# Performance work log

Hardware: AMD Instinct MI355X
Metric: run time of the kernel (lower is better)

Reference implementation:

```python
import jax, jax.numpy as jnp
import numpy as np
from jax import lax

B, C_IN, C_OUT, KS, K, FD, L = 32, 128, 256, 9, 8, 64, 4096
PAD = KS // 2


def setup_inputs() -> dict:
    key = jax.random.key(0)
    ks = jax.random.split(key, 8)
    X = jax.random.normal(ks[0], (B, C_IN, L), dtype=jnp.float32)
    Z = jax.random.normal(ks[1], (B, FD), dtype=jnp.float32)
    # z_to_in: Linear(fluct_dim, in_planes), xavier-ish init, zero bias
    z_in_w = jax.random.normal(ks[2], (C_IN, FD), dtype=jnp.float32) * (1.0 / np.sqrt(FD))
    z_in_b = jnp.zeros((C_IN,), dtype=jnp.float32)
    # z_to_w MLP: in_planes -> in_planes//2 -> K
    w1 = jax.random.normal(ks[3], (C_IN // 2, C_IN), dtype=jnp.float32) * (1.0 / np.sqrt(C_IN))
    b1 = jax.random.normal(ks[4], (C_IN // 2,), dtype=jnp.float32) * 0.01
    w2 = jax.random.normal(ks[5], (K, C_IN // 2), dtype=jnp.float32) * (1.0 / np.sqrt(C_IN // 2))
    b2 = jax.random.normal(ks[6], (K,), dtype=jnp.float32) * 0.01
    weight_bank = jax.random.normal(ks[7], (K, C_OUT, C_IN, KS), dtype=jnp.float32) * (1.0 / np.sqrt(C_IN * KS))
    bias_bank = jnp.zeros((K, C_OUT), dtype=jnp.float32)
    return {"X": X, "Z": Z, "z_in_w": z_in_w, "z_in_b": z_in_b,
            "w1": w1, "b1": b1, "w2": w2, "b2": b2,
            "weight_bank": weight_bank, "bias_bank": bias_bank}


def _conv_one(x, w):
    # x: (C_in, L); w: (C_out, C_in, KS) -> (C_out, L)
    y = lax.conv_general_dilated(x[None], w, window_strides=(1,),
                                 padding=[(PAD, PAD)],
                                 dimension_numbers=("NCH", "OIH", "NCH"))
    return y[0]


def reference(X, Z, z_in_w, z_in_b, w1, b1, w2, b2, weight_bank, bias_bank):
    # routing: Z -> in_planes -> MLP -> softmax over K (dropout is inference no-op)
    proj = Z @ z_in_w.T + z_in_b                       # (B, C_in)
    h = jax.nn.relu(proj @ w1.T + b1)                  # (B, C_in//2)
    logits = h @ w2.T + b2                             # (B, K)
    omega = jax.nn.softmax(logits, axis=1)             # (B, K)
    # per-sample mixed kernels and biases
    W_tilde = jnp.einsum("bk,koci->boci", omega, weight_bank)  # (B, C_out, C_in, KS)
    b_tilde = omega @ bias_bank                         # (B, C_out)
    # batched per-sample conv (equiv. of the groups=B conv1d trick)
    Y = jax.vmap(_conv_one)(X, W_tilde)                 # (B, C_out, L)
    return Y + b_tilde[:, :, None]
```

## Files before the change

kernel.cpp:

```cpp
#include <hip/hip_runtime.h>
#include <math.h>

#define B_     32
#define C_INP  128
#define C_OUTP 256
#define KS_    9
#define KK_    8
#define FD_    64
#define LL_    4096
#define PAD_   4

#define LPAD   (LL_ + 2 * PAD_)

typedef unsigned short ushort_t;
typedef short bf16x8 __attribute__((ext_vector_type(8)));
typedef float f32x4 __attribute__((ext_vector_type(4)));

__device__ __forceinline__ ushort_t f2bf(float f) {
    unsigned u = __float_as_uint(f);
    unsigned r = (u + 0x7FFFu + ((u >> 16) & 1u)) >> 16;
    return (ushort_t)r;
}

__device__ __forceinline__ void gload16(const void* g, void* l) {
    __builtin_amdgcn_global_load_lds(
        (const __attribute__((address_space(1))) unsigned int*)g,
        (__attribute__((address_space(3))) unsigned int*)l, 16, 0, 0);
}

__global__ __launch_bounds__(256) void routing_kernel(
    const float* __restrict__ Z, const float* __restrict__ z_in_w,
    const float* __restrict__ z_in_b, const float* __restrict__ w1,
    const float* __restrict__ b1, const float* __restrict__ w2,
    const float* __restrict__ b2, const float* __restrict__ bias_bank,
    float* __restrict__ omega_out, float* __restrict__ btilde_out)
{
    const int b = blockIdx.x;
    const int tid = threadIdx.x;
    __shared__ float s_z[FD_];
    __shared__ float s_proj[C_INP];
    __shared__ float s_h[FD_];
    __shared__ float s_logits[KK_];
    __shared__ float s_omega[KK_];

    if (tid < FD_) s_z[tid] = Z[b * FD_ + tid];
    __syncthreads();

    if (tid < C_INP) {
        float acc = z_in_b[tid];
        const float* w = z_in_w + tid * FD_;
        #pragma unroll 8
        for (int f = 0; f < FD_; ++f) acc = fmaf(w[f], s_z[f], acc);
        s_proj[tid] = acc;
    }
    __syncthreads();

    if (tid < FD_) {
        float acc = b1[tid];
        const float* w = w1 + tid * C_INP;
        #pragma unroll 8
        for (int c = 0; c < C_INP; ++c) acc = fmaf(w[c], s_proj[c], acc);
        s_h[tid] = fmaxf(acc, 0.0f);
    }
    __syncthreads();

    if (tid < KK_) {
        float acc = b2[tid];
        const float* w = w2 + tid * FD_;
        #pragma unroll 8
        for (int j = 0; j < FD_; ++j) acc = fmaf(w[j], s_h[j], acc);
        s_logits[tid] = acc;
    }
    __syncthreads();

    if (tid == 0) {
        float m = s_logits[0];
        #pragma unroll
        for (int k = 1; k < KK_; ++k) m = fmaxf(m, s_logits[k]);
        float e[KK_];
        float s = 0.0f;
        #pragma unroll
        for (int k = 0; k < KK_; ++k) { e[k] = expf(s_logits[k] - m); s += e[k]; }
        const float inv = 1.0f / s;
        #pragma unroll
        for (int k = 0; k < KK_; ++k) s_omega[k] = e[k] * inv;
    }
    __syncthreads();

    if (tid < KK_) omega_out[b * KK_ + tid] = s_omega[tid];

    {
        float acc = 0.0f;
        #pragma unroll
        for (int k = 0; k < KK_; ++k) acc = fmaf(s_omega[k], bias_bank[k * C_OUTP + tid], acc);
        btilde_out[b * C_OUTP + tid] = acc;
    }
}

__global__ __launch_bounds__(256) void mix_kernel(
    const float* __restrict__ bank, const float* __restrict__ omega,
    ushort_t* __restrict__ wt)
{
    __shared__ float s_bank[KK_ * C_INP * KS_];
    __shared__ float s_om[B_ * KK_];

    const int o = blockIdx.x;
    const int tid = threadIdx.x;

    s_om[tid] = omega[tid];
    #pragma unroll
    for (int k = 0; k < KK_; ++k) {
        const float* src = bank + ((size_t)(k * C_OUTP + o)) * (C_INP * KS_);
        for (int i = tid; i < C_INP * KS_; i += 256)
            s_bank[k * (C_INP * KS_) + i] = src[i];
    }
    __syncthreads();

    for (int j = tid; j < KS_ * (C_INP / 2); j += 256) {
        const int t = j >> 6;
        const int c = (j & 63) * 2;
        float v0[KK_], v1[KK_];
        #pragma unroll
        for (int k = 0; k < KK_; ++k) {
            v0[k] = s_bank[k * (C_INP * KS_) + c * KS_ + t];
            v1[k] = s_bank[k * (C_INP * KS_) + (c + 1) * KS_ + t];
        }
        #pragma unroll
        for (int b = 0; b < B_; ++b) {
            float a0 = 0.0f, a1 = 0.0f;
            #pragma unroll
            for (int k = 0; k < KK_; ++k) {
                const float om = s_om[b * KK_ + k];
                a0 = fmaf(om, v0[k], a0);
                a1 = fmaf(om, v1[k], a1);
            }
            const unsigned packed = (unsigned)f2bf(a0) | ((unsigned)f2bf(a1) << 16);
            *(unsigned*)&wt[(((size_t)b * KS_ + t) * C_OUTP + o) * C_INP + c] = packed;
        }
    }
}

__global__ __launch_bounds__(256) void transpose_kernel(
    const float* __restrict__ X, ushort_t* __restrict__ XT)
{
    __shared__ ushort_t s_t[64 * 130];

    const int tid = threadIdx.x;
    const int l0 = blockIdx.x * 64;
    const int b = blockIdx.y;

    const int ll = tid & 63;
    const int cq = tid >> 6;
    const float* xb = X + ((size_t)b * C_INP) * LL_;

    #pragma unroll 4
    for (int r = 0; r < 32; ++r) {
        const int c = r * 4 + cq;
        s_t[ll * 130 + c] = f2bf(xb[(size_t)c * LL_ + l0 + ll]);
    }
    __syncthreads();

    ushort_t* xtb = XT + (size_t)b * LPAD * C_INP;
    for (int it = tid; it < 64 * 64; it += 256) {
        const int row = it >> 6;
        const int p = it & 63;
        const unsigned lo = s_t[row * 130 + p * 2];
        const unsigned hi = s_t[row * 130 + p * 2 + 1];
        *(unsigned*)(xtb + ((size_t)(4 + l0 + row)) * C_INP + p * 2) = lo | (hi << 16);
    }
    if (l0 == 0) {
        const int row = tid >> 6, p = tid & 63;
        *(unsigned*)(xtb + (size_t)row * C_INP + p * 2) = 0u;
    }
    if (l0 == LL_ - 64) {
        const int row = tid >> 6, p = tid & 63;
        *(unsigned*)(xtb + ((size_t)(LL_ + PAD_ + row)) * C_INP + p * 2) = 0u;
    }
}

__global__ __launch_bounds__(256) void gemm_kernel(
    const ushort_t* __restrict__ XT, const ushort_t* __restrict__ WT,
    const float* __restrict__ btilde, float* __restrict__ Y)
{
    __shared__ __align__(16) ushort_t sX[136 * 128];
    __shared__ __align__(16) ushort_t sW[128 * 128];

    const int tid = threadIdx.x;
    const int wid = tid >> 6;
    const int lane = tid & 63;

    const int wg = blockIdx.x;
    const int logical = (wg & 7) * 256 + (wg >> 3);
    const int b  = logical >> 6;
    const int rem = logical & 63;
    const int o0 = (rem >> 5) << 7;
    const int l0 = (rem & 31) << 7;

    const int prow = lane >> 4;
    const int pcol = lane & 15;

    const ushort_t* xsrc = XT + ((size_t)b * LPAD + l0) * C_INP;
    for (int ci = wid; ci < 34; ci += 4) {
        const int row = ci * 4 + prow;
        const int scol = pcol ^ (row & 7);
        gload16(xsrc + row * C_INP + scol * 8, sX + ci * 512 + lane * 8);
    }

    {
        const ushort_t* wsrc = WT + (((size_t)b * KS_ + 0) * C_OUTP + o0) * C_INP;
        for (int ci = wid; ci < 32; ci += 4) {
            const int row = ci * 4 + prow;
            const int scol = pcol ^ (row & 7);
            gload16(wsrc + row * C_INP + scol * 8, sW + ci * 512 + lane * 8);
        }
    }
    __syncthreads();

    const int ln15 = lane & 15;
    const int lh = lane >> 4;
    const int wm0 = (wid >> 1) * 64;
    const int wn0 = (wid & 1) * 64;

    f32x4 acc[4][4];
    #pragma unroll
    for (int i = 0; i < 4; ++i)
        #pragma unroll
        for (int j = 0; j < 4; ++j) acc[i][j] = (f32x4){0.f, 0.f, 0.f, 0.f};

    for (int t = 0; t < KS_; ++t) {
        const int xrow0 = wn0 + t + ln15;
        #pragma unroll
        for (int kk = 0; kk < 4; ++kk) {
            const int col16 = kk * 4 + lh;
            bf16x8 a[4], bx[4];
            #pragma unroll
            for (int i = 0; i < 4; ++i) {
                const int arow = wm0 + i * 16 + ln15;
                a[i] = *(const bf16x8*)&sW[(arow << 7) + ((col16 ^ (arow & 7)) << 3)];
            }
            #pragma unroll
            for (int j = 0; j < 4; ++j) {
                const int brow = xrow0 + j * 16;
                bx[j] = *(const bf16x8*)&sX[(brow << 7) + ((col16 ^ (brow & 7)) << 3)];
            }
            #pragma unroll
            for (int i = 0; i < 4; ++i)
                #pragma unroll
                for (int j = 0; j < 4; ++j)
                    acc[i][j] = __builtin_amdgcn_mfma_f32_16x16x32_bf16(
                        a[i], bx[j], acc[i][j], 0, 0, 0);
        }
        __syncthreads();
        if (t < KS_ - 1) {
            const ushort_t* wsrc = WT + (((size_t)b * KS_ + (t + 1)) * C_OUTP + o0) * C_INP;
            for (int ci = wid; ci < 32; ci += 4) {
                const int row = ci * 4 + prow;
                const int scol = pcol ^ (row & 7);
                gload16(wsrc + row * C_INP + scol * 8, sW + ci * 512 + lane * 8);
            }
            __syncthreads();
        }
    }

    #pragma unroll
    for (int i = 0; i < 4; ++i) {
        const int obase = o0 + wm0 + i * 16 + lh * 4;
        const float4 bt = *(const float4*)&btilde[b * C_OUTP + obase];
        #pragma unroll
        for (int j = 0; j < 4; ++j) {
            const int lcol = l0 + wn0 + j * 16 + ln15;
            float* yp = Y + ((size_t)(b * C_OUTP + obase)) * LL_ + lcol;
            yp[0]           = acc[i][j][0] + bt.x;
            yp[LL_]         = acc[i][j][1] + bt.y;
            yp[2 * LL_]     = acc[i][j][2] + bt.z;
            yp[3 * LL_]     = acc[i][j][3] + bt.w;
        }
    }
}

#define O_TILE 8
#define T_PAD  12
__global__ __launch_bounds__(256) void conv_kernel(
    const float* __restrict__ X, const float* __restrict__ bank,
    const float* __restrict__ omega, const float* __restrict__ btilde,
    float* __restrict__ Y)
{
    __shared__ __align__(16) float s_w[C_INP * O_TILE * T_PAD];
    __shared__ float s_om[KK_];

    const int tid = threadIdx.x;
    const int o_base = blockIdx.x * O_TILE;
    const int b = blockIdx.y;

    if (tid < KK_) s_om[tid] = omega[b * KK_ + tid];
    __syncthreads();

    {
        const size_t kstride = (size_t)C_OUTP * C_INP * KS_;
        const float* bank_base = bank + (size_t)o_base * C_INP * KS_;
        for (int idx = tid; idx < O_TILE * C_INP * KS_; idx += 256) {
            const int o = idx / (C_INP * KS_);
            const int rem = idx - o * (C_INP * KS_);
            const int c = rem / KS_;
            const int t = rem - c * KS_;
            const float* p = bank_base + idx;
            float acc = 0.0f;
            #pragma unroll
            for (int k = 0; k < KK_; ++k) acc = fmaf(s_om[k], p[k * kstride], acc);
            s_w[(c * O_TILE + o) * T_PAD + t] = acc;
        }
    }
    __syncthreads();

    const int og = tid >> 7;
    const int lg = tid & 127;
    const float* xb = X + (size_t)b * C_INP * LL_;

    float bt[4];
    #pragma unroll
    for (int o = 0; o < 4; ++o) bt[o] = btilde[b * C_OUTP + o_base + og * 4 + o];

    for (int it = 0; it < 4; ++it) {
        const int l0 = it * 1024 + lg * 8;
        const int lx = l0 - PAD_;
        const bool fast = (lx >= 0) && (lx + 16 <= LL_);

        float acc[4][8];
        #pragma unroll
        for (int o = 0; o < 4; ++o)
            #pragma unroll
            for (int j = 0; j < 8; ++j) acc[o][j] = 0.0f;

        #pragma unroll 1
        for (int c = 0; c < C_INP; ++c) {
            const float* xrow = xb + (size_t)c * LL_;
            float x[16];
            if (fast) {
                const float4* p = reinterpret_cast<const float4*>(xrow + lx);
                const float4 a0 = p[0], a1 = p[1], a2 = p[2], a3 = p[3];
                x[0]=a0.x; x[1]=a0.y; x[2]=a0.z; x[3]=a0.w;
                x[4]=a1.x; x[5]=a1.y; x[6]=a1.z; x[7]=a1.w;
                x[8]=a2.x; x[9]=a2.y; x[10]=a2.z; x[11]=a2.w;
                x[12]=a3.x; x[13]=a3.y; x[14]=a3.z; x[15]=a3.w;
            } else {
                #pragma unroll
                for (int j = 0; j < 16; ++j) {
                    const int q = lx + j;
                    x[j] = (q >= 0 && q < LL_) ? xrow[q] : 0.0f;
                }
            }
            const float* wp = &s_w[(c * O_TILE + og * 4) * T_PAD];
            #pragma unroll
            for (int o = 0; o < 4; ++o) {
                #pragma unroll
                for (int t = 0; t < KS_; ++t) {
                    const float wv = wp[o * T_PAD + t];
                    #pragma unroll
                    for (int j = 0; j < 8; ++j)
                        acc[o][j] = fmaf(wv, x[j + t], acc[o][j]);
                }
            }
        }

        float* yb = Y + ((size_t)(b * C_OUTP + o_base + og * 4)) * LL_ + l0;
        #pragma unroll
        for (int o = 0; o < 4; ++o) {
            float4 r0, r1;
            r0.x = acc[o][0] + bt[o]; r0.y = acc[o][1] + bt[o];
            r0.z = acc[o][2] + bt[o]; r0.w = acc[o][3] + bt[o];
            r1.x = acc[o][4] + bt[o]; r1.y = acc[o][5] + bt[o];
            r1.z = acc[o][6] + bt[o]; r1.w = acc[o][7] + bt[o];
            float4* yp = reinterpret_cast<float4*>(yb + (size_t)o * LL_);
            yp[0] = r0; yp[1] = r1;
        }
    }
}

extern "C" void kernel_launch(void* const* d_in, const int* in_sizes, int n_in,
                              void* d_out, int out_size, void* d_ws, size_t ws_size,
                              hipStream_t stream)
{
    const float* X         = (const float*)d_in[0];
    const float* Z         = (const float*)d_in[1];
    const float* z_in_w    = (const float*)d_in[2];
    const float* z_in_b    = (const float*)d_in[3];
    const float* w1        = (const float*)d_in[4];
    const float* b1        = (const float*)d_in[5];
    const float* w2        = (const float*)d_in[6];
    const float* b2        = (const float*)d_in[7];
    const float* bank      = (const float*)d_in[8];
    const float* bias_bank = (const float*)d_in[9];
    float* out = (float*)d_out;

    char* ws = (char*)d_ws;
    float* omega  = (float*)ws;
    float* btilde = (float*)(ws + 1024);
    ushort_t* wt  = (ushort_t*)(ws + 1024 + 32768);
    ushort_t* XT  = (ushort_t*)(ws + 1024 + 32768 + (size_t)B_ * KS_ * C_OUTP * C_INP * 2);
    const size_t WS_NEEDED = 1024 + 32768
        + (size_t)B_ * KS_ * C_OUTP * C_INP * 2
        + (size_t)B_ * LPAD * C_INP * 2;

    routing_kernel<<<B_, 256, 0, stream>>>(Z, z_in_w, z_in_b, w1, b1, w2, b2,
                                           bias_bank, omega, btilde);

    if (ws_size >= WS_NEEDED) {
        mix_kernel<<<C_OUTP, 256, 0, stream>>>(bank, omega, wt);
        transpose_kernel<<<dim3(LL_ / 64, B_), 256, 0, stream>>>(X, XT);
        gemm_kernel<<<2048, 256, 0, stream>>>(XT, wt, btilde, out);
    } else {
        dim3 grid(C_OUTP / O_TILE, B_);
        conv_kernel<<<grid, 256, 0, stream>>>(X, bank, omega, btilde, out);
    }
}
```

Baseline: 136.4 us.

## Enlarge GEMM tile to 256x256 with double-buffered K-split weight loads

The implicit-GEMM conv kernel now uses 512-thread workgroups, each covering all 256 output channels by 256 positions, with a wave tile of 128x64. The reduction over input channels is split into two 64-wide halves, and the weight slice for the next step is prefetched into a second LDS buffer while the current step runs its MFMAs, which removes one barrier per tap. It also raises wave priority around the MFMA blocks. The aim is better data reuse and hiding load latency, at the cost of more accumulator registers (128 floats per lane), more LDS and fewer workgroups (512).

```diff
diff --git a/kernel.cpp b/kernel.cpp
--- a/kernel.cpp
+++ b/kernel.cpp
@@ -178,93 +178,112 @@
     }
 }
 
-__global__ __launch_bounds__(256) void gemm_kernel(
+__global__ __launch_bounds__(512, 2) void gemm_kernel(
     const ushort_t* __restrict__ XT, const ushort_t* __restrict__ WT,
     const float* __restrict__ btilde, float* __restrict__ Y)
 {
-    __shared__ __align__(16) ushort_t sX[136 * 128];
-    __shared__ __align__(16) ushort_t sW[128 * 128];
+    __shared__ __align__(16) ushort_t sW[2][256 * 64];
+    __shared__ __align__(16) ushort_t sX[2][264 * 64];
 
     const int tid = threadIdx.x;
     const int wid = tid >> 6;
     const int lane = tid & 63;
 
     const int wg = blockIdx.x;
-    const int logical = (wg & 7) * 256 + (wg >> 3);
-    const int b  = logical >> 6;
-    const int rem = logical & 63;
-    const int o0 = (rem >> 5) << 7;
-    const int l0 = (rem & 31) << 7;
-
-    const int prow = lane >> 4;
-    const int pcol = lane & 15;
-
-    const ushort_t* xsrc = XT + ((size_t)b * LPAD + l0) * C_INP;
-    for (int ci = wid; ci < 34; ci += 4) {
-        const int row = ci * 4 + prow;
-        const int scol = pcol ^ (row & 7);
-        gload16(xsrc + row * C_INP + scol * 8, sX + ci * 512 + lane * 8);
-    }
+    const int logical = (wg & 7) * 64 + (wg >> 3);
+    const int b  = logical >> 4;
+    const int l0 = (logical & 15) << 8;
 
     {
-        const ushort_t* wsrc = WT + (((size_t)b * KS_ + 0) * C_OUTP + o0) * C_INP;
-        for (int ci = wid; ci < 32; ci += 4) {
-            const int row = ci * 4 + prow;
-            const int scol = pcol ^ (row & 7);
-            gload16(wsrc + row * C_INP + scol * 8, sW + ci * 512 + lane * 8);
+        const ushort_t* xtb = XT + ((size_t)b * LPAD + l0) * C_INP;
+        #pragma unroll
+        for (int g0 = 0; g0 < 4224; g0 += 512) {
+            const int g = g0 + tid;
+            if (g < 4224) {
+                const int ch = g / 2112;
+                const int gg = g - ch * 2112;
+                const int row = gg >> 3;
+                const int pc = gg & 7;
+                const int scol = pc ^ (row & 7);
+                gload16(xtb + row * C_INP + ch * 64 + scol * 8,
+                        &sX[ch][0] + gg * 8);
+            }
+        }
+        const ushort_t* wbase = WT + (((size_t)b * KS_ + 0) * C_OUTP) * C_INP;
+        #pragma unroll
+        for (int it = 0; it < 4; ++it) {
+            const int g = it * 512 + tid;
+            const int row = g >> 3;
+            const int pc = g & 7;
+            const int scol = pc ^ (row & 7);
+            gload16(wbase + row * C_INP + scol * 8, &sW[0][0] + g * 8);
         }
     }
     __syncthreads();
 
     const int ln15 = lane & 15;
     const int lh = lane >> 4;
-    const int wm0 = (wid >> 1) * 64;
-    const int wn0 = (wid & 1) * 64;
-
-    f32x4 acc[4][4];
+    const int wm0 = (wid >> 2) * 128;
+    const int wn0 = (wid & 3) * 64;
+
+    f32x4 acc[8][4];
     #pragma unroll
-    for (int i = 0; i < 4; ++i)
+    for (int i = 0; i < 8; ++i)
         #pragma unroll
         for (int j = 0; j < 4; ++j) acc[i][j] = (f32x4){0.f, 0.f, 0.f, 0.f};
 
-    for (int t = 0; t < KS_; ++t) {
-        const int xrow0 = wn0 + t + ln15;
-        #pragma unroll
-        for (int kk = 0; kk < 4; ++kk) {
-            const int col16 = kk * 4 + lh;
-            bf16x8 a[4], bx[4];
-            #pragma unroll
-            for (int i = 0; i < 4; ++i) {
+    #pragma unroll 1
+    for (int s = 0; s < 2 * KS_; ++s) {
+        const int buf = s & 1;
+        const int t = s >> 1;
+        const int ch = s & 1;
+
+        if (s < 2 * KS_ - 1) {
+            const int s1 = s + 1;
+            const int t1 = s1 >> 1;
+            const int ch1 = s1 & 1;
+            const ushort_t* wbase =
+                WT + (((size_t)b * KS_ + t1) * C_OUTP) * C_INP + ch1 * 64;
+            #pragma unroll
+            for (int it = 0; it < 4; ++it) {
+                const int g = it * 512 + tid;
+                const int row = g >> 3;
+                const int pc = g & 7;
+                const int scol = pc ^ (row & 7);
+                gload16(wbase + row * C_INP + scol * 8, &sW[buf ^ 1][0] + g * 8);
+            }
+        }
+
+        const ushort_t* wh = &sW[buf][0];
+        const ushort_t* xh = &sX[ch][0];
+        #pragma unroll
+        for (int kk = 0; kk < 2; ++kk) {
+            bf16x8 a[8], bx[4];
+            #pragma unroll
+            for (int i = 0; i < 8; ++i) {
                 const int arow = wm0 + i * 16 + ln15;
-                a[i] = *(const bf16x8*)&sW[(arow << 7) + ((col16 ^ (arow & 7)) << 3)];
+                a[i] = *(const bf16x8*)&wh[arow * 64 + (((kk * 4 + lh) ^ (arow & 7)) << 3)];
             }
             #pragma unroll
             for (int j = 0; j < 4; ++j) {
-                const int brow = xrow0 + j * 16;
-                bx[j] = *(const bf16x8*)&sX[(brow << 7) + ((col16 ^ (brow & 7)) << 3)];
-            }
-            #pragma unroll
-            for (int i = 0; i < 4; ++i)
+                const int brow = wn0 + t + j * 16 + ln15;
+                bx[j] = *(const bf16x8*)&xh[brow * 64 + (((kk * 4 + lh) ^ (brow & 7)) << 3)];
+            }
+            __builtin_amdgcn_s_setprio(1);
+            #pragma unroll
+            for (int i = 0; i < 8; ++i)
                 #pragma unroll
                 for (int j = 0; j < 4; ++j)
                     acc[i][j] = __builtin_amdgcn_mfma_f32_16x16x32_bf16(
                         a[i], bx[j], acc[i][j], 0, 0, 0);
+            __builtin_amdgcn_s_setprio(0);
         }
         __syncthreads();
-        if (t < KS_ - 1) {
-            const ushort_t* wsrc = WT + (((size_t)b * KS_ + (t + 1)) * C_OUTP + o0) * C_INP;
-            for (int ci = wid; ci < 32; ci += 4) {
-                const int row = ci * 4 + prow;
-                const int scol = pcol ^ (row & 7);
-                gload16(wsrc + row * C_INP + scol * 8, sW + ci * 512 + lane * 8);
-            }
-            __syncthreads();
-        }
     }
 
     #pragma unroll
-    for (int i = 0; i < 4; ++i) {
-        const int obase = o0 + wm0 + i * 16 + lh * 4;
+    for (int i = 0; i < 8; ++i) {
+        const int obase = wm0 + i * 16 + lh * 4;
         const float4 bt = *(const float4*)&btilde[b * C_OUTP + obase];
         #pragma unroll
         for (int j = 0; j < 4; ++j) {
@@ -407,7 +426,7 @@
     if (ws_size >= WS_NEEDED) {
         mix_kernel<<<C_OUTP, 256, 0, stream>>>(bank, omega, wt);
         transpose_kernel<<<dim3(LL_ / 64, B_), 256, 0, stream>>>(X, XT);
-        gemm_kernel<<<2048, 256, 0, stream>>>(XT, wt, btilde, out);
+        gemm_kernel<<<512, 512, 0, stream>>>(XT, wt, btilde, out);
     } else {
         dim3 grid(C_OUTP / O_TILE, B_);
         conv_kernel<<<grid, 256, 0, stream>>>(X, bank, omega, btilde, out);
```

Result: no change. 137.1 us (+0.5%).

## Pipeline weight tiles through a four-slot LDS ring with prefetch depth three

Applied to the files above, without the earlier changes.

The weight tile is now split into 32-channel K-slices held in a four-slot shared-memory ring. Each loop step prefetches the slice three steps ahead with async global-to-LDS loads while MFMAs run on the current slice. This replaces the serial load/sync/compute per tap and its double barrier with one barrier plus a partial vmcnt wait. It also sets launch bounds for two blocks per CU, raises wave priority around the MFMA block, and uses a new swizzle for the narrower weight layout. The risk is correctness of the hand-written waitcnt/barrier ordering, and the wrap-around prefetch loads redundant data at the end of the loop.

```diff
diff --git a/kernel.cpp b/kernel.cpp
--- a/kernel.cpp
+++ b/kernel.cpp
@@ -178,12 +178,12 @@
     }
 }
 
-__global__ __launch_bounds__(256) void gemm_kernel(
+__global__ __launch_bounds__(256, 2) void gemm_kernel(
     const ushort_t* __restrict__ XT, const ushort_t* __restrict__ WT,
     const float* __restrict__ btilde, float* __restrict__ Y)
 {
     __shared__ __align__(16) ushort_t sX[136 * 128];
-    __shared__ __align__(16) ushort_t sW[128 * 128];
+    __shared__ __align__(16) ushort_t sWr[4][128 * 32];
 
     const int tid = threadIdx.x;
     const int wid = tid >> 6;
@@ -196,22 +196,24 @@
     const int o0 = (rem >> 5) << 7;
     const int l0 = (rem & 31) << 7;
 
-    const int prow = lane >> 4;
-    const int pcol = lane & 15;
-
-    const ushort_t* xsrc = XT + ((size_t)b * LPAD + l0) * C_INP;
-    for (int ci = wid; ci < 34; ci += 4) {
-        const int row = ci * 4 + prow;
-        const int scol = pcol ^ (row & 7);
-        gload16(xsrc + row * C_INP + scol * 8, sX + ci * 512 + lane * 8);
-    }
-
-    {
-        const ushort_t* wsrc = WT + (((size_t)b * KS_ + 0) * C_OUTP + o0) * C_INP;
-        for (int ci = wid; ci < 32; ci += 4) {
-            const int row = ci * 4 + prow;
-            const int scol = pcol ^ (row & 7);
-            gload16(wsrc + row * C_INP + scol * 8, sW + ci * 512 + lane * 8);
+    const ushort_t* xtb = XT + ((size_t)b * LPAD + l0) * C_INP;
+    const ushort_t* wtb = WT + ((size_t)b * KS_ * C_OUTP + o0) * C_INP;
+
+    for (int g = tid; g < 2176; g += 256) {
+        const int row = g >> 4;
+        const int pcp = g & 15;
+        gload16(xtb + row * C_INP + ((pcp ^ (row & 7)) * 8), sX + g * 8);
+    }
+    #pragma unroll
+    for (int p = 0; p < 3; ++p) {
+        ushort_t* wd = sWr[p];
+        #pragma unroll
+        for (int itr = 0; itr < 2; ++itr) {
+            const int g = itr * 256 + tid;
+            const int row = g >> 2;
+            const int sp = g & 3;
+            gload16(wtb + row * C_INP + p * 32 + ((sp ^ ((row >> 1) & 3)) * 8),
+                    wd + g * 8);
         }
     }
     __syncthreads();
@@ -227,40 +229,50 @@
         #pragma unroll
         for (int j = 0; j < 4; ++j) acc[i][j] = (f32x4){0.f, 0.f, 0.f, 0.f};
 
-    for (int t = 0; t < KS_; ++t) {
-        const int xrow0 = wn0 + t + ln15;
-        #pragma unroll
-        for (int kk = 0; kk < 4; ++kk) {
-            const int col16 = kk * 4 + lh;
-            bf16x8 a[4], bx[4];
+    #pragma unroll 1
+    for (int s = 0; s < 36; ++s) {
+        const int t = s >> 2;
+        const int q = s & 3;
+        int s3 = s + 3; if (s3 >= 36) s3 -= 36;
+        const ushort_t* wr = sWr[s & 3];
+        ushort_t* wdst = sWr[s3 & 3];
+        const ushort_t* wsrc = wtb + (size_t)(s3 >> 2) * (C_OUTP * C_INP) + (s3 & 3) * 32;
+
+        bf16x8 a[4], bx[4];
+        #pragma unroll
+        for (int i = 0; i < 4; ++i) {
+            const int arow = wm0 + i * 16 + ln15;
+            a[i] = *(const bf16x8*)&sWr[s & 3][arow * 32 + ((lh ^ ((arow >> 1) & 3)) << 3)];
+        }
+        #pragma unroll
+        for (int j = 0; j < 4; ++j) {
+            const int brow = wn0 + t + j * 16 + ln15;
+            bx[j] = *(const bf16x8*)&sX[brow * 128 + (((q * 4 + lh) ^ (brow & 7)) << 3)];
+        }
+        (void)wr;
+
+        #pragma unroll
+        for (int itr = 0; itr < 2; ++itr) {
+            const int g = itr * 256 + tid;
+            const int row = g >> 2;
+            const int sp = g & 3;
+            gload16(wsrc + row * C_INP + ((sp ^ ((row >> 1) & 3)) * 8), wdst + g * 8);
+        }
+
+        __builtin_amdgcn_s_setprio(1);
+        #pragma unroll
+        for (int i = 0; i < 4; ++i)
             #pragma unroll
-            for (int i = 0; i < 4; ++i) {
-                const int arow = wm0 + i * 16 + ln15;
-                a[i] = *(const bf16x8*)&sW[(arow << 7) + ((col16 ^ (arow & 7)) << 3)];
-            }
-            #pragma unroll
-            for (int j = 0; j < 4; ++j) {
-                const int brow = xrow0 + j * 16;
-                bx[j] = *(const bf16x8*)&sX[(brow << 7) + ((col16 ^ (brow & 7)) << 3)];
-            }
-            #pragma unroll
-            for (int i = 0; i < 4; ++i)
-                #pragma unroll
-                for (int j = 0; j < 4; ++j)
-                    acc[i][j] = __builtin_amdgcn_mfma_f32_16x16x32_bf16(
-                        a[i], bx[j], acc[i][j], 0, 0, 0);
-        }
-        __syncthreads();
-        if (t < KS_ - 1) {
-            const ushort_t* wsrc = WT + (((size_t)b * KS_ + (t + 1)) * C_OUTP + o0) * C_INP;
-            for (int ci = wid; ci < 32; ci += 4) {
-                const int row = ci * 4 + prow;
-                const int scol = pcol ^ (row & 7);
-                gload16(wsrc + row * C_INP + scol * 8, sW + ci * 512 + lane * 8);
-            }
-            __syncthreads();
-        }
-    }
+            for (int j = 0; j < 4; ++j)
+                acc[i][j] = __builtin_amdgcn_mfma_f32_16x16x32_bf16(
+                    a[i], bx[j], acc[i][j], 0, 0, 0);
+        __builtin_amdgcn_s_setprio(0);
+
+        asm volatile("s_waitcnt vmcnt(4)" ::: "memory");
+        __builtin_amdgcn_s_barrier();
+        __builtin_amdgcn_sched_barrier(0);
+    }
+    asm volatile("s_waitcnt vmcnt(0)" ::: "memory");
 
     #pragma unroll
     for (int i = 0; i < 4; ++i) {
```

Measured after the change: 127.5 us. -6.5%, faster.
